# Optimization experiments

Measured on AMD Instinct MI355X. Metric: run time of the kernel, lower is better.

Reference implementation:

```python
import jax, jax.numpy as jnp
import numpy as np

NUM_HEADS = 16
HIDDEN = 1024
HEAD_DIM = HIDDEN // NUM_HEADS
B, S, D = 2, 2048, 1024


def setup_inputs() -> dict:
    key = jax.random.key(0)
    ks = jax.random.split(key, 7)
    scale = 1.0 / np.sqrt(D)
    return {
        "query": jax.random.normal(ks[0], (B, S, D), dtype=jnp.float32),
        "key": jax.random.normal(ks[1], (B, S, D), dtype=jnp.float32),
        "value": jax.random.normal(ks[2], (B, S, D), dtype=jnp.float32),
        "Wk_w": jax.random.normal(ks[3], (HIDDEN, D), dtype=jnp.float32) * scale,
        "Wk_b": jax.random.normal(ks[4], (HIDDEN,), dtype=jnp.float32) * scale,
        "Wv_w": jax.random.normal(ks[5], (HIDDEN, D), dtype=jnp.float32) * scale,
        "Wv_b": jax.random.normal(ks[6], (HIDDEN,), dtype=jnp.float32) * scale,
    }


def reference(query, key, value, Wk_w, Wk_b, Wv_w, Wv_b):
    # NOTE: in the original torch module, self.W_v is assigned twice, so the
    # SAME Linear (Wv) projects both key and value; Wk projects query.
    b, s, _ = query.shape

    def split_heads(x):  # [b,s,hidden] -> [b,h,s,hd]
        return x.reshape(b, s, NUM_HEADS, HEAD_DIM).transpose(0, 2, 1, 3)

    q = split_heads(query @ Wk_w.T + Wk_b)
    k = split_heads(key @ Wv_w.T + Wv_b)
    v = split_heads(value @ Wv_w.T + Wv_b)

    scores = jnp.einsum("bhqd,bhkd->bhqk", q, k) / jnp.sqrt(
        jnp.asarray(HEAD_DIM, dtype=q.dtype))
    probs = jax.nn.softmax(scores, axis=-1)
    out = jnp.einsum("bhqk,bhkd->bhqd", probs, v)
    return out.transpose(0, 2, 1, 3).reshape(b, s, NUM_HEADS * HEAD_DIM)
```

## Files before the change

kernel.cpp:

```cpp
#include <hip/hip_runtime.h>
#include <stdint.h>

typedef unsigned short u16;
typedef uint32_t u32;
typedef __bf16 bf16x8 __attribute__((ext_vector_type(8)));
typedef float f32x4 __attribute__((ext_vector_type(4)));
typedef u16 u16x4 __attribute__((ext_vector_type(4)));
typedef u16 u16x8 __attribute__((ext_vector_type(8)));

#define XQ_OFF 0ul
#define XK_OFF 4194304ul
#define XV_OFF 8388608ul
#define WK_OFF 12582912ul
#define WV_OFF 13631488ul
#define Q_OFF  14680064ul
#define K_OFF  18874368ul
#define V_OFF  23068672ul

#define SCQ 0.18033688011112042f

#if __has_builtin(__builtin_amdgcn_exp2f)
#define EXP2F(x) __builtin_amdgcn_exp2f(x)
#else
#define EXP2F(x) exp2f(x)
#endif

__device__ __forceinline__ u16 f2bf(float f) {
  u32 u = __float_as_uint(f);
  u32 r = (u + 0x7fffu + ((u >> 16) & 1u)) >> 16;
  return (u16)r;
}

__device__ __forceinline__ u32 pk2(float a, float b) {
  typedef __bf16 bf2_t __attribute__((ext_vector_type(2)));
  typedef float f2_t __attribute__((ext_vector_type(2)));
  f2_t v; v[0] = a; v[1] = b;
  bf2_t h = __builtin_convertvector(v, bf2_t);
  union { bf2_t h; u32 u; } cv; cv.h = h; return cv.u;
}

__device__ __forceinline__ void load_lds16(const void* g, void* l) {
  __builtin_amdgcn_global_load_lds(
      (const __attribute__((address_space(1))) u32*)g,
      (__attribute__((address_space(3))) u32*)l, 16, 0, 0);
}

__device__ __forceinline__ u32 swz(u32 L) {
  return L ^ (((L >> 7) & 1u) << 4) ^ (((L >> 10) & 3u) << 5);
}

__global__ __launch_bounds__(256) void cvt_tile_kernel(
    const float* __restrict__ xq, const float* __restrict__ xk,
    const float* __restrict__ xv, const float* __restrict__ wk,
    const float* __restrict__ wv, u16* __restrict__ ws) {
  __shared__ u16 tile[4096];
  const int bid = blockIdx.x;
  const float* src; size_t dstbase; int rt, ktp;
  if (bid < 3072) {
    int m = bid >> 10, loc = bid & 1023;
    src = (m == 0) ? xq : (m == 1) ? xk : xv;
    dstbase = (size_t)m * 4194304ul;
    rt = loc >> 4; ktp = loc & 15;
  } else {
    int r2 = bid - 3072;
    int m = r2 >> 8, loc = r2 & 255;
    src = m ? wv : wk;
    dstbase = WK_OFF + (size_t)m * 1048576ul;
    rt = loc >> 4; ktp = loc & 15;
  }
  const int t = threadIdx.x;
  const int row0 = t >> 4, c = t & 15;
  const int k = c * 4;
  const float* s = src + (size_t)(rt * 64 + row0) * 1024ul + ktp * 64 + k;
#pragma unroll
  for (int i = 0; i < 4; ++i) {
    float4 v = *(const float4*)(s + (size_t)i * 16384ul);
    int row = row0 + i * 16;
    u32* p = (u32*)(tile + ((k >> 5) * 2048 + ((k >> 3) & 3) * 512 + row * 8 + (k & 7)));
    p[0] = pk2(v.x, v.y);
    p[1] = pk2(v.z, v.w);
  }
  __syncthreads();
  u16* dst = ws + dstbase + (size_t)(rt * 32 + ktp * 2) * 2048ul;
#pragma unroll
  for (int so = 0; so < 4096; so += 2048)
    *(u16x8*)(dst + so + t * 8) = *(const u16x8*)(tile + so + t * 8);
}

__global__ __launch_bounds__(256, 3) void proj_kernel(u16* __restrict__ ws,
                                                      const float* __restrict__ bk,
                                                      const float* __restrict__ bv) {
  const int proj = blockIdx.z;
  const int mtile = blockIdx.x;
  const int ntile = blockIdx.y;
  const u16* A = ws + (size_t)proj * 4194304ul;
  const u16* Bw = ws + ((proj == 0) ? WK_OFF : WV_OFF);
  const float* bias = (proj == 0) ? bk : bv;
  u16* outQ = ws + Q_OFF;
  u16* outK = ws + K_OFF;
  u16* outV = ws + V_OFF;

  const int t = threadIdx.x;
  const int w = t >> 6, lane = t & 63;
  const int wm = w >> 1, wn = w & 1;
  const int g = lane >> 4, c = lane & 15;

  __shared__ __align__(16) u16 smem[24576];

  const u16* Ag = A + (size_t)(2 * mtile) * 65536ul;
  const u16* Bg = Bw + (size_t)(2 * ntile) * 65536ul;
  const u32 t8 = (u32)t * 8u;
  const u32 so = swz((u32)t * 16u) >> 1;

  u32 poff[4];
#pragma unroll
  for (int mt = 0; mt < 4; ++mt)
    poff[mt] = swz((u32)((g << 10) | ((mt * 16 + c) << 4))) >> 1;

#define PSTAGE(buf, kt)                                            \
  do {                                                             \
    u16* bb = smem + (buf) * 8192;                                 \
    const size_t ko = (size_t)(kt) * 2048ul + so;                  \
    load_lds16(Ag + ko, bb + t8);                                  \
    load_lds16(Ag + 65536ul + ko, bb + 2048 + t8);                 \
    load_lds16(Bg + ko, bb + 4096 + t8);                           \
    load_lds16(Bg + 65536ul + ko, bb + 6144 + t8);                 \
  } while (0)

#define PFRAGS_MFMA(buf)                                                        \
  do {                                                                          \
    const u16* Ap = smem + (buf) * 8192 + wm * 2048;                            \
    const u16* Bp = smem + (buf) * 8192 + 4096 + wn * 2048;                     \
    bf16x8 af[4], bfv[4];                                                       \
    _Pragma("unroll") for (int mt = 0; mt < 4; ++mt)                            \
        af[mt] = *(const bf16x8*)(Ap + poff[mt]);                               \
    _Pragma("unroll") for (int nt = 0; nt < 4; ++nt)                            \
        bfv[nt] = *(const bf16x8*)(Bp + poff[nt]);                              \
    _Pragma("unroll") for (int mt = 0; mt < 4; ++mt)                            \
        _Pragma("unroll") for (int nt = 0; nt < 4; ++nt)                        \
            acc[mt][nt] = __builtin_amdgcn_mfma_f32_16x16x32_bf16(              \
                af[mt], bfv[nt], acc[mt][nt], 0, 0, 0);                         \
  } while (0)

  f32x4 acc[4][4];
#pragma unroll
  for (int mt = 0; mt < 4; ++mt)
#pragma unroll
    for (int nt = 0; nt < 4; ++nt) acc[mt][nt] = (f32x4){0.f, 0.f, 0.f, 0.f};

  PSTAGE(0, 0);
  PSTAGE(1, 1);

  int cur = 0, stg = 2;
#pragma unroll 1
  for (int kt = 0; kt < 31; ++kt) {
    asm volatile("s_waitcnt vmcnt(4)\n\ts_barrier" ::: "memory");
    if (kt < 30) PSTAGE(stg, kt + 2);
    PFRAGS_MFMA(cur);
    cur = (cur == 2) ? 0 : cur + 1;
    stg = (stg == 2) ? 0 : stg + 1;
  }
  asm volatile("s_waitcnt vmcnt(0)\n\ts_barrier" ::: "memory");
  PFRAGS_MFMA(cur);
#undef PSTAGE
#undef PFRAGS_MFMA

  const int m0 = mtile * 128 + wm * 64;
  const int n0 = ntile * 128 + wn * 64;
  if (proj == 2) {
#pragma unroll
    for (int nt = 0; nt < 4; ++nt) {
      const int col = n0 + nt * 16 + c;
      const float bvv = bias[col];
      const int h = col >> 6, d = col & 63;
#pragma unroll
      for (int mt = 0; mt < 4; ++mt) {
        const int mbase = m0 + mt * 16 + g * 4;
        const int b = mbase >> 11;
        const int bh = b * 16 + h;
        const int s = mbase & 2047;
        u16x4 pk;
#pragma unroll
        for (int r = 0; r < 4; ++r) pk[r] = f2bf(acc[mt][nt][r] + bvv);
        size_t idx = (size_t)bh * 131072ul + (size_t)(s >> 6) * 4096ul +
                     (size_t)((s & 63) >> 3) * 512ul + (size_t)d * 8ul + (size_t)(s & 7);
        *(u16x4*)(outV + idx) = pk;
      }
    }
  } else {
    __syncthreads();
    u16* Ew = smem + w * 4096;
#pragma unroll
    for (int nt = 0; nt < 4; ++nt) {
      const int d = nt * 16 + c;
      const float bvv = bias[n0 + nt * 16 + c];
#pragma unroll
      for (int mt = 0; mt < 4; ++mt) {
#pragma unroll
        for (int r = 0; r < 4; ++r) {
          const int srow = mt * 16 + g * 4 + r;
          float y = acc[mt][nt][r] + bvv;
          if (proj == 0) y *= SCQ;
          Ew[(d >> 3) * 512 + srow * 8 + (d & 7)] = f2bf(y);
        }
      }
    }
    __syncthreads();
    const int b = mtile >> 4;
    const int bh = b * 16 + ntile * 2 + wn;
    if (proj == 0) {
      u16* base = outQ + (size_t)bh * 131072ul + (size_t)(mtile & 15) * 8192ul + wm * 512;
#pragma unroll
      for (int i = 0; i < 8; ++i)
        *(u16x8*)(base + i * 1024 + lane * 8) = *(const u16x8*)(Ew + i * 512 + lane * 8);
    } else {
      u16* base = outK + (size_t)bh * 131072ul + (size_t)((mtile & 15) * 2 + wm) * 4096ul;
#pragma unroll
      for (int i = 0; i < 8; ++i)
        *(u16x8*)(base + i * 512 + lane * 8) = *(const u16x8*)(Ew + i * 512 + lane * 8);
    }
  }
}

__device__ __forceinline__ void attn_step(
    int jj, const u16* __restrict__ Kg, const u16* __restrict__ Vg,
    bf16x8 (&kf)[2][4], bf16x8 (&vcur)[2][4], bf16x8 (&vnxt)[2][4],
    const bf16x8 (&qf)[2][2], const bf16x8 onesf, f32x4 (&O)[2][4],
    f32x4 (&Lacc)[2], u16* __restrict__ Psw, int g, int c) {
  const int jn = (jj < 31) ? jj + 1 : 31;
  const u16* Vn = Vg + (size_t)jn * 4096ul;
#pragma unroll
  for (int ksh = 0; ksh < 2; ++ksh)
#pragma unroll
    for (int nt = 0; nt < 4; ++nt)
      vnxt[ksh][nt] = *(const bf16x8*)(Vn + (ksh * 4 + g) * 512 + (nt * 16 + c) * 8);

  f32x4 St[4][2];
#pragma unroll
  for (int mtk = 0; mtk < 4; ++mtk)
#pragma unroll
    for (int ntq = 0; ntq < 2; ++ntq) St[mtk][ntq] = (f32x4){0.f, 0.f, 0.f, 0.f};
  __builtin_amdgcn_s_setprio(1);
#pragma unroll
  for (int ks = 0; ks < 2; ++ks)
#pragma unroll
    for (int mtk = 0; mtk < 4; ++mtk)
#pragma unroll
      for (int ntq = 0; ntq < 2; ++ntq)
        St[mtk][ntq] =
            __builtin_amdgcn_mfma_f32_16x16x32_bf16(kf[ks][mtk], qf[ntq][ks], St[mtk][ntq], 0, 0, 0);
  __builtin_amdgcn_s_setprio(0);

  const u16* Kn = Kg + (size_t)jn * 4096ul;
#pragma unroll
  for (int ks = 0; ks < 2; ++ks)
#pragma unroll
    for (int mtk = 0; mtk < 4; ++mtk)
      kf[ks][mtk] = *(const bf16x8*)(Kn + (ks * 4 + g) * 512 + (mtk * 16 + c) * 8);

#pragma unroll
  for (int mtk = 0; mtk < 4; ++mtk)
#pragma unroll
    for (int ntq = 0; ntq < 2; ++ntq)
#pragma unroll
      for (int r = 0; r < 4; ++r) St[mtk][ntq][r] = EXP2F(St[mtk][ntq][r]);

#pragma unroll
  for (int ksh = 0; ksh < 2; ++ksh) {
#pragma unroll
    for (int ntq = 0; ntq < 2; ++ntq)
#pragma unroll
      for (int m2 = 0; m2 < 2; ++m2) {
        const int mtk = ksh * 2 + m2;
        u32 lo = pk2(St[mtk][ntq][0], St[mtk][ntq][1]);
        u32 hi = pk2(St[mtk][ntq][2], St[mtk][ntq][3]);
        u32* p = (u32*)(Psw + (ntq * 16 + c) * 40 + m2 * 16 + g * 4);
        p[0] = lo; p[1] = hi;
      }
    asm volatile("s_waitcnt lgkmcnt(0)" ::: "memory");
    bf16x8 pf[2];
#pragma unroll
    for (int mtq = 0; mtq < 2; ++mtq)
      pf[mtq] = *(const bf16x8*)(Psw + (mtq * 16 + c) * 40 + g * 8);
    __builtin_amdgcn_s_setprio(1);
#pragma unroll
    for (int mtq = 0; mtq < 2; ++mtq) {
      Lacc[mtq] = __builtin_amdgcn_mfma_f32_16x16x32_bf16(pf[mtq], onesf, Lacc[mtq], 0, 0, 0);
#pragma unroll
      for (int nt = 0; nt < 4; ++nt)
        O[mtq][nt] =
            __builtin_amdgcn_mfma_f32_16x16x32_bf16(pf[mtq], vcur[ksh][nt], O[mtq][nt], 0, 0, 0);
    }
    __builtin_amdgcn_s_setprio(0);
  }
}

__global__ __launch_bounds__(256, 2) void attn_kernel(const u16* __restrict__ ws,
                                                      float* __restrict__ out) {
  const int bh = blockIdx.x, qtile = blockIdx.y;
  const int b = bh >> 4, h = bh & 15;
  const int t = threadIdx.x, w = t >> 6, lane = t & 63, g = lane >> 4, c = lane & 15;

  __shared__ __align__(16) u16 Ps[4][1280];

  const u16* Qg = ws + Q_OFF + (size_t)bh * 131072ul + (size_t)qtile * 8192ul;
  const u16* Kg = ws + K_OFF + (size_t)bh * 131072ul;
  const u16* Vg = ws + V_OFF + (size_t)bh * 131072ul;

  bf16x8 qf[2][2];
#pragma unroll
  for (int ntq = 0; ntq < 2; ++ntq)
#pragma unroll
    for (int ks = 0; ks < 2; ++ks)
      qf[ntq][ks] = *(const bf16x8*)(Qg + (ks * 4 + g) * 1024 + (w * 32 + ntq * 16 + c) * 8);

  u16x8 ou;
#pragma unroll
  for (int i = 0; i < 8; ++i) ou[i] = (u16)0x3F80;
  union { u16x8 u; bf16x8 b; } ocv; ocv.u = ou;
  const bf16x8 onesf = ocv.b;

  f32x4 O[2][4], Lacc[2];
#pragma unroll
  for (int mtq = 0; mtq < 2; ++mtq) {
    Lacc[mtq] = (f32x4){0.f, 0.f, 0.f, 0.f};
#pragma unroll
    for (int nt = 0; nt < 4; ++nt) O[mtq][nt] = (f32x4){0.f, 0.f, 0.f, 0.f};
  }

  u16* Psw = Ps[w];

  bf16x8 kf[2][4];
#pragma unroll
  for (int ks = 0; ks < 2; ++ks)
#pragma unroll
    for (int mtk = 0; mtk < 4; ++mtk)
      kf[ks][mtk] = *(const bf16x8*)(Kg + (ks * 4 + g) * 512 + (mtk * 16 + c) * 8);
  bf16x8 vfA[2][4], vfB[2][4];
#pragma unroll
  for (int ksh = 0; ksh < 2; ++ksh)
#pragma unroll
    for (int nt = 0; nt < 4; ++nt)
      vfA[ksh][nt] = *(const bf16x8*)(Vg + (ksh * 4 + g) * 512 + (nt * 16 + c) * 8);

#pragma unroll 1
  for (int j2 = 0; j2 < 16; ++j2) {
    attn_step(2 * j2, Kg, Vg, kf, vfA, vfB, qf, onesf, O, Lacc, Psw, g, c);
    attn_step(2 * j2 + 1, Kg, Vg, kf, vfB, vfA, qf, onesf, O, Lacc, Psw, g, c);
  }

  const int q0 = qtile * 128 + w * 32;
#pragma unroll
  for (int mtq = 0; mtq < 2; ++mtq)
#pragma unroll
    for (int r = 0; r < 4; ++r) {
      const float inv = 1.0f / Lacc[mtq][r];
      const int q = q0 + mtq * 16 + g * 4 + r;
      float* rowp = out + (size_t)(b * 2048 + q) * 1024ul + h * 64;
#pragma unroll
      for (int nt = 0; nt < 4; ++nt) rowp[nt * 16 + c] = O[mtq][nt][r] * inv;
    }
}

extern "C" void kernel_launch(void* const* d_in, const int* in_sizes, int n_in,
                              void* d_out, int out_size, void* d_ws, size_t ws_size,
                              hipStream_t stream) {
  const float* q = (const float*)d_in[0];
  const float* k = (const float*)d_in[1];
  const float* v = (const float*)d_in[2];
  const float* wk = (const float*)d_in[3];
  const float* bk = (const float*)d_in[4];
  const float* wv = (const float*)d_in[5];
  const float* bv = (const float*)d_in[6];
  u16* ws = (u16*)d_ws;
  float* out = (float*)d_out;

  cvt_tile_kernel<<<3584, 256, 0, stream>>>(q, k, v, wk, wv, ws);
  proj_kernel<<<dim3(32, 8, 3), 256, 0, stream>>>(ws, bk, bv);
  attn_kernel<<<dim3(32, 16), 256, 0, stream>>>(ws, out);
}
```

Baseline: 175.5 us.

## Stage K/V tiles in LDS with triple buffering and use 32x32 MFMA

Rewrites the attention kernel so K and V tiles are loaded asynchronously into a three-deep shared-memory ring shared by all four waves, instead of each wave loading its own register fragments from global memory. Scores and PV use 32x32x16 bf16 MFMAs, and P is kept in registers via v_permlane32_swap instead of a round trip through LDS. The row-sum is now accumulated with vector adds and reduced at the end with a permlane swap and ds_bpermute. This cuts duplicate global traffic and LDS P shuffles, but adds a barrier per tile and more LDS pressure.

New measurement: 177.1 us. About the same (+0.9%).

```diff
diff --git a/kernel.cpp b/kernel.cpp
--- a/kernel.cpp
+++ b/kernel.cpp
@@ -5,6 +5,7 @@
 typedef uint32_t u32;
 typedef __bf16 bf16x8 __attribute__((ext_vector_type(8)));
 typedef float f32x4 __attribute__((ext_vector_type(4)));
+typedef float f32x16 __attribute__((ext_vector_type(16)));
 typedef u16 u16x4 __attribute__((ext_vector_type(4)));
 typedef u16 u16x8 __attribute__((ext_vector_type(8)));
 
@@ -222,144 +223,126 @@
   }
 }
 
-__device__ __forceinline__ void attn_step(
-    int jj, const u16* __restrict__ Kg, const u16* __restrict__ Vg,
-    bf16x8 (&kf)[2][4], bf16x8 (&vcur)[2][4], bf16x8 (&vnxt)[2][4],
-    const bf16x8 (&qf)[2][2], const bf16x8 onesf, f32x4 (&O)[2][4],
-    f32x4 (&Lacc)[2], u16* __restrict__ Psw, int g, int c) {
-  const int jn = (jj < 31) ? jj + 1 : 31;
-  const u16* Vn = Vg + (size_t)jn * 4096ul;
-#pragma unroll
-  for (int ksh = 0; ksh < 2; ++ksh)
-#pragma unroll
-    for (int nt = 0; nt < 4; ++nt)
-      vnxt[ksh][nt] = *(const bf16x8*)(Vn + (ksh * 4 + g) * 512 + (nt * 16 + c) * 8);
-
-  f32x4 St[4][2];
-#pragma unroll
-  for (int mtk = 0; mtk < 4; ++mtk)
-#pragma unroll
-    for (int ntq = 0; ntq < 2; ++ntq) St[mtk][ntq] = (f32x4){0.f, 0.f, 0.f, 0.f};
-  __builtin_amdgcn_s_setprio(1);
-#pragma unroll
-  for (int ks = 0; ks < 2; ++ks)
-#pragma unroll
-    for (int mtk = 0; mtk < 4; ++mtk)
-#pragma unroll
-      for (int ntq = 0; ntq < 2; ++ntq)
-        St[mtk][ntq] =
-            __builtin_amdgcn_mfma_f32_16x16x32_bf16(kf[ks][mtk], qf[ntq][ks], St[mtk][ntq], 0, 0, 0);
-  __builtin_amdgcn_s_setprio(0);
-
-  const u16* Kn = Kg + (size_t)jn * 4096ul;
-#pragma unroll
-  for (int ks = 0; ks < 2; ++ks)
-#pragma unroll
-    for (int mtk = 0; mtk < 4; ++mtk)
-      kf[ks][mtk] = *(const bf16x8*)(Kn + (ks * 4 + g) * 512 + (mtk * 16 + c) * 8);
-
-#pragma unroll
-  for (int mtk = 0; mtk < 4; ++mtk)
-#pragma unroll
-    for (int ntq = 0; ntq < 2; ++ntq)
-#pragma unroll
-      for (int r = 0; r < 4; ++r) St[mtk][ntq][r] = EXP2F(St[mtk][ntq][r]);
-
-#pragma unroll
-  for (int ksh = 0; ksh < 2; ++ksh) {
-#pragma unroll
-    for (int ntq = 0; ntq < 2; ++ntq)
-#pragma unroll
-      for (int m2 = 0; m2 < 2; ++m2) {
-        const int mtk = ksh * 2 + m2;
-        u32 lo = pk2(St[mtk][ntq][0], St[mtk][ntq][1]);
-        u32 hi = pk2(St[mtk][ntq][2], St[mtk][ntq][3]);
-        u32* p = (u32*)(Psw + (ntq * 16 + c) * 40 + m2 * 16 + g * 4);
-        p[0] = lo; p[1] = hi;
-      }
-    asm volatile("s_waitcnt lgkmcnt(0)" ::: "memory");
-    bf16x8 pf[2];
-#pragma unroll
-    for (int mtq = 0; mtq < 2; ++mtq)
-      pf[mtq] = *(const bf16x8*)(Psw + (mtq * 16 + c) * 40 + g * 8);
-    __builtin_amdgcn_s_setprio(1);
-#pragma unroll
-    for (int mtq = 0; mtq < 2; ++mtq) {
-      Lacc[mtq] = __builtin_amdgcn_mfma_f32_16x16x32_bf16(pf[mtq], onesf, Lacc[mtq], 0, 0, 0);
-#pragma unroll
-      for (int nt = 0; nt < 4; ++nt)
-        O[mtq][nt] =
-            __builtin_amdgcn_mfma_f32_16x16x32_bf16(pf[mtq], vcur[ksh][nt], O[mtq][nt], 0, 0, 0);
-    }
-    __builtin_amdgcn_s_setprio(0);
-  }
-}
-
 __global__ __launch_bounds__(256, 2) void attn_kernel(const u16* __restrict__ ws,
                                                       float* __restrict__ out) {
   const int bh = blockIdx.x, qtile = blockIdx.y;
   const int b = bh >> 4, h = bh & 15;
-  const int t = threadIdx.x, w = t >> 6, lane = t & 63, g = lane >> 4, c = lane & 15;
-
-  __shared__ __align__(16) u16 Ps[4][1280];
+  const int t = threadIdx.x, w = t >> 6, lane = t & 63;
+  const int c32 = lane & 31, g2 = lane >> 5;
+
+  __shared__ __align__(16) u16 Ks[3][4096];
+  __shared__ __align__(16) u16 Vs[3][4096];
 
   const u16* Qg = ws + Q_OFF + (size_t)bh * 131072ul + (size_t)qtile * 8192ul;
   const u16* Kg = ws + K_OFF + (size_t)bh * 131072ul;
   const u16* Vg = ws + V_OFF + (size_t)bh * 131072ul;
 
-  bf16x8 qf[2][2];
-#pragma unroll
-  for (int ntq = 0; ntq < 2; ++ntq)
-#pragma unroll
-    for (int ks = 0; ks < 2; ++ks)
-      qf[ntq][ks] = *(const bf16x8*)(Qg + (ks * 4 + g) * 1024 + (w * 32 + ntq * 16 + c) * 8);
-
-  u16x8 ou;
-#pragma unroll
-  for (int i = 0; i < 8; ++i) ou[i] = (u16)0x3F80;
-  union { u16x8 u; bf16x8 b; } ocv; ocv.u = ou;
-  const bf16x8 onesf = ocv.b;
-
-  f32x4 O[2][4], Lacc[2];
-#pragma unroll
-  for (int mtq = 0; mtq < 2; ++mtq) {
-    Lacc[mtq] = (f32x4){0.f, 0.f, 0.f, 0.f};
-#pragma unroll
-    for (int nt = 0; nt < 4; ++nt) O[mtq][nt] = (f32x4){0.f, 0.f, 0.f, 0.f};
-  }
-
-  u16* Psw = Ps[w];
-
-  bf16x8 kf[2][4];
-#pragma unroll
-  for (int ks = 0; ks < 2; ++ks)
-#pragma unroll
-    for (int mtk = 0; mtk < 4; ++mtk)
-      kf[ks][mtk] = *(const bf16x8*)(Kg + (ks * 4 + g) * 512 + (mtk * 16 + c) * 8);
-  bf16x8 vfA[2][4], vfB[2][4];
-#pragma unroll
-  for (int ksh = 0; ksh < 2; ++ksh)
-#pragma unroll
-    for (int nt = 0; nt < 4; ++nt)
-      vfA[ksh][nt] = *(const bf16x8*)(Vg + (ksh * 4 + g) * 512 + (nt * 16 + c) * 8);
-
+  bf16x8 qf[4];
+#pragma unroll
+  for (int ks = 0; ks < 4; ++ks)
+    qf[ks] = *(const bf16x8*)(Qg + (size_t)(ks * 2 + g2) * 1024ul +
+                              (size_t)(w * 32 + c32) * 8ul);
+
+  f32x16 O0, O1, Lacc;
+#pragma unroll
+  for (int i = 0; i < 16; ++i) { O0[i] = 0.f; O1[i] = 0.f; Lacc[i] = 0.f; }
+
+#define STAGE_KV(buf, jj)                                        \
+  do {                                                           \
+    const u16* Kj = Kg + (size_t)(jj) * 4096ul;                  \
+    const u16* Vj = Vg + (size_t)(jj) * 4096ul;                  \
+    load_lds16(Kj + (size_t)t * 8ul, &Ks[buf][t * 8]);           \
+    load_lds16(Kj + 2048ul + (size_t)t * 8ul, &Ks[buf][2048 + t * 8]); \
+    load_lds16(Vj + (size_t)t * 8ul, &Vs[buf][t * 8]);           \
+    load_lds16(Vj + 2048ul + (size_t)t * 8ul, &Vs[buf][2048 + t * 8]); \
+  } while (0)
+
+  STAGE_KV(0, 0);
+  STAGE_KV(1, 1);
+
+  int buf = 0;
 #pragma unroll 1
-  for (int j2 = 0; j2 < 16; ++j2) {
-    attn_step(2 * j2, Kg, Vg, kf, vfA, vfB, qf, onesf, O, Lacc, Psw, g, c);
-    attn_step(2 * j2 + 1, Kg, Vg, kf, vfB, vfA, qf, onesf, O, Lacc, Psw, g, c);
-  }
+  for (int j = 0; j < 32; ++j) {
+    asm volatile("s_waitcnt vmcnt(4)\n\ts_barrier" ::: "memory");
+    const u16* Kb = Ks[buf];
+    const u16* Vb = Vs[buf];
+    {
+      int jc = (j + 2 < 32) ? j + 2 : 31;
+      int sb = buf - 1; if (sb < 0) sb += 3;
+      STAGE_KV(sb, jc);
+    }
+
+    f32x16 S0, S1;
+#pragma unroll
+    for (int i = 0; i < 16; ++i) { S0[i] = 0.f; S1[i] = 0.f; }
+    __builtin_amdgcn_s_setprio(1);
+#pragma unroll
+    for (int ks = 0; ks < 4; ++ks) {
+      bf16x8 kf0 = *(const bf16x8*)(Kb + (ks * 2 + g2) * 512 + c32 * 8);
+      bf16x8 kf1 = *(const bf16x8*)(Kb + (ks * 2 + g2) * 512 + (32 + c32) * 8);
+      S0 = __builtin_amdgcn_mfma_f32_32x32x16_bf16(kf0, qf[ks], S0, 0, 0, 0);
+      S1 = __builtin_amdgcn_mfma_f32_32x32x16_bf16(kf1, qf[ks], S1, 0, 0, 0);
+    }
+    __builtin_amdgcn_s_setprio(0);
+
+#pragma unroll
+    for (int i = 0; i < 16; ++i) { S0[i] = EXP2F(S0[i]); S1[i] = EXP2F(S1[i]); }
+    Lacc += S0;
+    Lacc += S1;
+
+    u32 pa[4][4];
+#pragma unroll
+    for (int half = 0; half < 2; ++half) {
+      const f32x16& Sx = half ? S1 : S0;
+#pragma unroll
+      for (int sub = 0; sub < 2; ++sub) {
+        const int rb = sub * 8;
+        u32 a0 = pk2(Sx[rb + 0], Sx[rb + 1]);
+        u32 a1 = pk2(Sx[rb + 2], Sx[rb + 3]);
+        u32 a2 = pk2(Sx[rb + 4], Sx[rb + 5]);
+        u32 a3 = pk2(Sx[rb + 6], Sx[rb + 7]);
+        asm volatile("v_permlane32_swap_b32 %0, %1" : "+v"(a0), "+v"(a2));
+        asm volatile("v_permlane32_swap_b32 %0, %1" : "+v"(a1), "+v"(a3));
+        const int kstep = half * 2 + sub;
+        pa[kstep][0] = a0; pa[kstep][1] = a1; pa[kstep][2] = a2; pa[kstep][3] = a3;
+      }
+    }
+
+    __builtin_amdgcn_s_setprio(1);
+#pragma unroll
+    for (int kstep = 0; kstep < 4; ++kstep) {
+      union { u32 u[4]; bf16x8 b; } pcv;
+#pragma unroll
+      for (int i = 0; i < 4; ++i) pcv.u[i] = pa[kstep][i];
+      bf16x8 vf0 = *(const bf16x8*)(Vb + (kstep * 2 + g2) * 512 + c32 * 8);
+      bf16x8 vf1 = *(const bf16x8*)(Vb + (kstep * 2 + g2) * 512 + (32 + c32) * 8);
+      O0 = __builtin_amdgcn_mfma_f32_32x32x16_bf16(pcv.b, vf0, O0, 0, 0, 0);
+      O1 = __builtin_amdgcn_mfma_f32_32x32x16_bf16(pcv.b, vf1, O1, 0, 0, 0);
+    }
+    __builtin_amdgcn_s_setprio(0);
+
+    buf = (buf == 2) ? 0 : buf + 1;
+  }
+#undef STAGE_KV
+
+  float lp = 0.f;
+#pragma unroll
+  for (int i = 0; i < 16; ++i) lp += Lacc[i];
+  float lA = lp, lB = lp;
+  asm volatile("v_permlane32_swap_b32 %0, %1" : "+v"(lA), "+v"(lB));
+  const float Ltot = lA + lB;
 
   const int q0 = qtile * 128 + w * 32;
-#pragma unroll
-  for (int mtq = 0; mtq < 2; ++mtq)
-#pragma unroll
-    for (int r = 0; r < 4; ++r) {
-      const float inv = 1.0f / Lacc[mtq][r];
-      const int q = q0 + mtq * 16 + g * 4 + r;
-      float* rowp = out + (size_t)(b * 2048 + q) * 1024ul + h * 64;
-#pragma unroll
-      for (int nt = 0; nt < 4; ++nt) rowp[nt * 16 + c] = O[mtq][nt][r] * inv;
-    }
+  float* outb = out + (size_t)(b * 2048 + q0) * 1024ul + h * 64 + c32;
+#pragma unroll
+  for (int r = 0; r < 16; ++r) {
+    const int qr = (r & 3) + 8 * (r >> 2) + 4 * g2;
+    int lv = __builtin_amdgcn_ds_bpermute(qr << 2, __float_as_int(Ltot));
+    const float inv = 1.0f / __int_as_float(lv);
+    float* rp = outb + (size_t)qr * 1024ul;
+    rp[0] = O0[r] * inv;
+    rp[32] = O1[r] * inv;
+  }
 }
 
 extern "C" void kernel_launch(void* const* d_in, const int* in_sizes, int n_in,
```
